# Kernel tuning notes

Measured on AMD Instinct MI355X. Metric: run time of the kernel, lower is better.

## Reference

```python
import jax, jax.numpy as jnp
import numpy as np

# Faithful JAX port of RayObsGraph.forward with T=1.
# torch_geometric GraphConv(x, edge_index) with add-aggregation and no edge
# weights computes: out[i] = lin_root(x[i]) + lin_rel(sum_{(j->i) in E} x[j]),
# where lin_root has no bias and lin_rel has a bias. dense_to_sparse(adj)
# yields an edge (row j -> col i) for every nonzero adj[j, i], so the
# aggregation equals binarize(adj)^T @ x, computed batched here instead of the
# original per-sample Python loop.

GS = 128      # graph_size
OBS = 1024    # obs_dim
H = 256       # gcn_h_size
OUT = 1024    # gcn_outsize
NO = 18       # num_outputs
B = 256

def setup_inputs() -> dict:
    key = jax.random.key(0)
    ks = jax.random.split(key, 16)
    inp = {
        "flat": jax.random.normal(ks[0], (B, OBS), jnp.float32),
        "nodes": jax.random.normal(ks[1], (B, GS, OBS), jnp.float32),
        "num_nodes": jax.random.randint(ks[2], (B,), 0, GS),
        "adj": jax.random.randint(ks[3], (B, GS, GS), 0, 2),
        "seq_lens": jnp.ones((B,), jnp.int32),
        # GraphConv 0: lin_rel (bias) + lin_root (no bias)
        "W0_rel": jax.random.normal(ks[4], (OBS, H), jnp.float32) / np.sqrt(OBS),
        "b0": jnp.zeros((H,), jnp.float32),
        "W0_root": jax.random.normal(ks[5], (OBS, H), jnp.float32) / np.sqrt(OBS),
        # GraphConv 1
        "W1_rel": jax.random.normal(ks[6], (H, OUT), jnp.float32) / np.sqrt(H),
        "b1": jnp.zeros((OUT,), jnp.float32),
        "W1_root": jax.random.normal(ks[7], (H, OUT), jnp.float32) / np.sqrt(H),
        # logit / value branches (SlimFC, activation None)
        "Wl": jax.random.normal(ks[8], (OUT, NO), jnp.float32) / np.sqrt(OUT),
        "bl": jnp.zeros((NO,), jnp.float32),
        "Wv": jax.random.normal(ks[9], (OUT, 1), jnp.float32) / np.sqrt(OUT),
        "bv": jnp.zeros((1,), jnp.float32),
    }
    return inp

def _forward(flat, nodes, adj, num_nodes,
             W0_rel, b0, W0_root, W1_rel, b1, W1_root, Wl, bl, Wv, bv):
    bsz = flat.shape[0]
    bi = jnp.arange(bsz)
    n = num_nodes
    nm1 = jnp.maximum(n - 1, 0)
    has_prev = n > 0

    # dense_to_sparse treats any nonzero entry as an edge (weight unused)
    A = (adj != 0).astype(flat.dtype)                       # [B, GS, GS]
    A = A.at[bi, n, n].set(1.0)
    A = A.at[bi, n, nm1].set(jnp.where(has_prev, 1.0, A[bi, n, nm1]))
    A = A.at[bi, nm1, n].set(jnp.where(has_prev, 1.0, A[bi, nm1, n]))

    # write current observation into node slot num_nodes
    x = nodes.at[bi, n].set(flat)                           # [B, GS, OBS]

    At = jnp.swapaxes(A, 1, 2)                              # message j->i: A^T
    aggr0 = jnp.einsum('bij,bjd->bid', At, x)               # [B, GS, OBS]
    h0 = jax.nn.relu(aggr0 @ W0_rel + b0 + x @ W0_root)     # [B, GS, H]
    aggr1 = jnp.einsum('bij,bjd->bid', At, h0)              # [B, GS, H]
    h1 = jax.nn.relu(aggr1 @ W1_rel + b1 + h0 @ W1_root)    # [B, GS, OUT]

    node_out = h1[bi, n]                                    # [B, OUT]
    logits = node_out @ Wl + bl                             # [B, NO]
    values = (node_out @ Wv + bv).squeeze(-1)               # [B]
    return logits, values

def reference(flat, nodes, num_nodes, adj, seq_lens,
              W0_rel, b0, W0_root, W1_rel, b1, W1_root, Wl, bl, Wv, bv):
    # seq_lens only determines B = len(seq_lens); T = flat.shape[0] // B = 1
    del seq_lens
    return _forward(flat, nodes, adj, num_nodes,
                    W0_rel, b0, W0_root, W1_rel, b1, W1_root, Wl, bl, Wv, bv)
```

## Files before the change

### kernel.cpp

```cpp
#include <hip/hip_runtime.h>
#include <hip/hip_bf16.h>
#include <cstdint>
#include <cstddef>

#define GS     128
#define OBS    1024
#define HSZ    256
#define OUTSZ  1024
#define NOUT   18
#define BATCH  256

typedef short  short8  __attribute__((ext_vector_type(8)));
typedef float  f32x4   __attribute__((ext_vector_type(4)));

__device__ __forceinline__ uint32_t f2bf_bits(float f) {
  uint32_t u = __builtin_bit_cast(uint32_t, f);
  return (u + 0x7fffu + ((u >> 16) & 1u)) >> 16;
}
__device__ __forceinline__ float bf_bits2f(uint32_t b) {
  return __builtin_bit_cast(float, b << 16);
}
__device__ __forceinline__ uint4 cvt8s(const float4 a, const float4 b) {
  float v[8] = {a.x, a.y, a.z, a.w, b.x, b.y, b.z, b.w};
  uint32_t h[8];
#pragma unroll
  for (int e = 0; e < 8; ++e) h[e] = f2bf_bits(v[e]);
  return make_uint4(h[0] | (h[1] << 16), h[2] | (h[3] << 16),
                    h[4] | (h[5] << 16), h[6] | (h[7] << 16));
}

__device__ __forceinline__ void bar_lds() {
  asm volatile("s_waitcnt lgkmcnt(0)" ::: "memory");
  __builtin_amdgcn_s_barrier();
  __builtin_amdgcn_sched_barrier(0);
}

__global__ __launch_bounds__(256) void prep_kernel(
    const float* __restrict__ W0_rel, const float* __restrict__ W0_root,
    ushort* __restrict__ WtP,
    const float* __restrict__ W1_rel, const float* __restrict__ W1_root,
    ushort* __restrict__ W1bf)
{
  __shared__ float T[64][65];
  const int blk = blockIdx.x;
  const int t = threadIdx.x;
  if (blk < 128) {
    const int k0 = (blk & 15) * 64;
    const int n0 = (blk >> 4) * 64;
    for (int idx = t; idx < 4096; idx += 256) {
      const int r = idx >> 6, c = idx & 63;
      const int n = n0 + c;
      T[r][c] = (n < HSZ) ? W0_rel[(size_t)(k0 + r) * HSZ + n]
                          : W0_root[(size_t)(k0 + r) * HSZ + (n - HSZ)];
    }
    __syncthreads();
    for (int idx = t; idx < 512; idx += 256) {
      const int nl = idx >> 3;
      const int kc = idx & 7;
      uint32_t h[8];
#pragma unroll
      for (int e = 0; e < 8; ++e) h[e] = f2bf_bits(T[kc * 8 + e][nl]);
      const int kg = k0 + kc * 8;
      const uint4 w = make_uint4(h[0] | (h[1] << 16), h[2] | (h[3] << 16),
                                 h[4] | (h[5] << 16), h[6] | (h[7] << 16));
      *(uint4*)&WtP[((size_t)((kg >> 5) * 512 + n0 + nl)) * 32 + (kg & 31)] = w;
    }
  } else {
    const int base = (blk - 128) * 16384;
    for (int it = 0; it < 64; ++it) {
      const int idx = base + it * 256 + t;
      const int k = idx >> 10, o = idx & 1023;
      const float v = (k < HSZ) ? W1_rel[(size_t)k * OUTSZ + o]
                                : W1_root[(size_t)(k - HSZ) * OUTSZ + o];
      W1bf[idx] = (ushort)f2bf_bits(v);
    }
  }
}

__global__ __launch_bounds__(512, 2) void mega_kernel(
    const float* __restrict__ flat, const float* __restrict__ nodes,
    const int* __restrict__ num_nodes, const int* __restrict__ adj,
    const float* __restrict__ b0, const ushort* __restrict__ WtP,
    ushort* __restrict__ zbf)
{
  __shared__ alignas(16) char smem[135168];
  ushort (*Ys)[264]      = (ushort (*)[264])smem;
  ushort (*As2)[128][72] = (ushort (*)[128][72])smem;
  __shared__ uint32_t rm[128][4];
  __shared__ uint32_t cmL[128][4];

  const int b  = blockIdx.x;
  const int nb = num_nodes[b];
  const int t  = threadIdx.x;
  const int wv = t >> 6, lane = t & 63;
  const int ln = lane & 15, q = lane >> 4;

  {
    const int* abase = adj + ((size_t)b * GS + wv * 16) * GS;
    int va[16], vb[16];
#pragma unroll
    for (int i = 0; i < 16; ++i) {
      va[i] = abase[i * GS + lane];
      vb[i] = abase[i * GS + 64 + lane];
    }
#pragma unroll
    for (int i = 0; i < 16; ++i) {
      const int k = wv * 16 + i;
      const unsigned long long m0 = __ballot(va[i] != 0);
      const unsigned long long m1 = __ballot(vb[i] != 0);
      if (lane == 0) {
        rm[k][0] = (uint32_t)m0; rm[k][1] = (uint32_t)(m0 >> 32);
        rm[k][2] = (uint32_t)m1; rm[k][3] = (uint32_t)(m1 >> 32);
      }
    }
  }
  __syncthreads();
  if (t < 128) {
    uint32_t c0 = 0, c1 = 0, c2 = 0, c3 = 0;
    const int w = t >> 5, sh = t & 31;
#pragma unroll 8
    for (int k = 0; k < 128; ++k) {
      const uint32_t bit = (rm[k][w] >> sh) & 1u;
      if (k < 32)      c0 |= bit << k;
      else if (k < 64) c1 |= bit << (k - 32);
      else if (k < 96) c2 |= bit << (k - 64);
      else             c3 |= bit << (k - 96);
    }
    cmL[t][0] = c0; cmL[t][1] = c1; cmL[t][2] = c2; cmL[t][3] = c3;
  }
  __syncthreads();
  if (t == 0) {
    cmL[nb][nb >> 5] |= 1u << (nb & 31);
    if (nb > 0) {
      cmL[nb - 1][nb >> 5] |= 1u << (nb & 31);
      cmL[nb][(nb - 1) >> 5] |= 1u << ((nb - 1) & 31);
    }
  }

  const int arow = t >> 2;
  const int akb  = (t & 3) * 16;
  const float* xsrc = ((arow == nb) ? (flat + (size_t)b * OBS)
                                    : (nodes + ((size_t)b * GS + arow) * OBS)) + akb;
  const ushort* bptr = WtP + ((size_t)(wv * 64 + ln)) * 32 + q * 8;

  f32x4 acc[4][8] = {};

  {
    const float4 a0 = *(const float4*)(xsrc);
    const float4 a1 = *(const float4*)(xsrc + 4);
    const float4 a2 = *(const float4*)(xsrc + 8);
    const float4 a3 = *(const float4*)(xsrc + 12);
    *(uint4*)&As2[0][arow][akb]     = cvt8s(a0, a1);
    *(uint4*)&As2[0][arow][akb + 8] = cvt8s(a2, a3);
  }
  float4 g0 = *(const float4*)(xsrc + 64);
  float4 g1 = *(const float4*)(xsrc + 68);
  float4 g2 = *(const float4*)(xsrc + 72);
  float4 g3 = *(const float4*)(xsrc + 76);
  short8 bA0 = *(const short8*)(bptr);
  short8 bA1 = *(const short8*)(bptr + 512);
  short8 bA2 = *(const short8*)(bptr + 1024);
  short8 bA3 = *(const short8*)(bptr + 1536);
  bar_lds();

  for (int s = 0; s < 16; ++s) {
    const int buf = s & 1;
    const ushort* bpB = bptr + ((size_t)(2 * s + 1)) * 16384;
    const short8 bB0 = *(const short8*)(bpB);
    const short8 bB1 = *(const short8*)(bpB + 512);
    const short8 bB2 = *(const short8*)(bpB + 1024);
    const short8 bB3 = *(const short8*)(bpB + 1536);
    short8 ah[8];
#pragma unroll
    for (int ii = 0; ii < 8; ++ii)
      ah[ii] = *(const short8*)&As2[buf][ii * 16 + ln][q * 8];
#pragma unroll
    for (int ii = 0; ii < 8; ++ii) {
      acc[0][ii] = __builtin_amdgcn_mfma_f32_16x16x32_bf16(bA0, ah[ii], acc[0][ii], 0, 0, 0);
      acc[1][ii] = __builtin_amdgcn_mfma_f32_16x16x32_bf16(bA1, ah[ii], acc[1][ii], 0, 0, 0);
      acc[2][ii] = __builtin_amdgcn_mfma_f32_16x16x32_bf16(bA2, ah[ii], acc[2][ii], 0, 0, 0);
      acc[3][ii] = __builtin_amdgcn_mfma_f32_16x16x32_bf16(bA3, ah[ii], acc[3][ii], 0, 0, 0);
    }
    short8 ah2[8];
#pragma unroll
    for (int ii = 0; ii < 8; ++ii)
      ah2[ii] = *(const short8*)&As2[buf][ii * 16 + ln][32 + q * 8];
    if (s + 1 < 16) {
      *(uint4*)&As2[buf ^ 1][arow][akb]     = cvt8s(g0, g1);
      *(uint4*)&As2[buf ^ 1][arow][akb + 8] = cvt8s(g2, g3);
    }
    short8 nA0 = {}, nA1 = {}, nA2 = {}, nA3 = {};
    if (s + 1 < 16) {
      const ushort* bpA = bptr + ((size_t)(2 * s + 2)) * 16384;
      nA0 = *(const short8*)(bpA);
      nA1 = *(const short8*)(bpA + 512);
      nA2 = *(const short8*)(bpA + 1024);
      nA3 = *(const short8*)(bpA + 1536);
    }
    if (s + 2 < 16) {
      g0 = *(const float4*)(xsrc + (s + 2) * 64);
      g1 = *(const float4*)(xsrc + (s + 2) * 64 + 4);
      g2 = *(const float4*)(xsrc + (s + 2) * 64 + 8);
      g3 = *(const float4*)(xsrc + (s + 2) * 64 + 12);
    }
#pragma unroll
    for (int ii = 0; ii < 8; ++ii) {
      acc[0][ii] = __builtin_amdgcn_mfma_f32_16x16x32_bf16(bB0, ah2[ii], acc[0][ii], 0, 0, 0);
      acc[1][ii] = __builtin_amdgcn_mfma_f32_16x16x32_bf16(bB1, ah2[ii], acc[1][ii], 0, 0, 0);
      acc[2][ii] = __builtin_amdgcn_mfma_f32_16x16x32_bf16(bB2, ah2[ii], acc[2][ii], 0, 0, 0);
      acc[3][ii] = __builtin_amdgcn_mfma_f32_16x16x32_bf16(bB3, ah2[ii], acc[3][ii], 0, 0, 0);
    }
    bA0 = nA0; bA1 = nA1; bA2 = nA2; bA3 = nA3;
    bar_lds();
  }

#pragma unroll
  for (int jj = 0; jj < 4; ++jj) {
    const int cat = wv * 64 + jj * 16 + q * 4;
    const int h   = cat & 255;
    const int kof = (cat < 256) ? 0 : 128;
#pragma unroll
    for (int ii = 0; ii < 8; ++ii) {
      const int kk = kof + ii * 16 + ln;
#pragma unroll
      for (int r = 0; r < 4; ++r)
        Ys[h + r][kk] = (ushort)f2bf_bits(acc[jj][ii][r]);
    }
  }
  __syncthreads();

  f32x4 acc2[8][2] = {};
#pragma unroll
  for (int ks = 0; ks < 4; ++ks) {
    const short8 bf0 = *(const short8*)&Ys[wv * 32 + ln][ks * 32 + q * 8];
    const short8 bf1 = *(const short8*)&Ys[wv * 32 + 16 + ln][ks * 32 + q * 8];
#pragma unroll
    for (int jt = 0; jt < 8; ++jt) {
      const uint32_t w = cmL[jt * 16 + ln][ks];
      const uint32_t byte_ = (w >> (q * 8)) & 0xFFu;
      short8 af;
#pragma unroll
      for (int i = 0; i < 8; ++i)
        af[i] = (short)(((byte_ >> i) & 1u) ? 0x3F80 : 0);
      acc2[jt][0] = __builtin_amdgcn_mfma_f32_16x16x32_bf16(af, bf0, acc2[jt][0], 0, 0, 0);
      acc2[jt][1] = __builtin_amdgcn_mfma_f32_16x16x32_bf16(af, bf1, acc2[jt][1], 0, 0, 0);
    }
  }

  const uint32_t S0 = cmL[nb][0], S1 = cmL[nb][1],
                 S2 = cmL[nb][2], S3 = cmL[nb][3];
  const int hl0 = wv * 32 + ln, hl1 = hl0 + 16;
  const float bb0 = b0[hl0];
  const float bb1 = b0[hl1];

  float asum0 = 0.f, asum1 = 0.f;
#pragma unroll
  for (int jt = 0; jt < 8; ++jt)
#pragma unroll
    for (int r = 0; r < 4; ++r) {
      const int j = jt * 16 + q * 4 + r;
      const uint32_t Sw = (j < 32) ? S0 : (j < 64) ? S1 : (j < 96) ? S2 : S3;
      const bool sj = (Sw >> (j & 31)) & 1u;
      const bool isn = (j == nb);
      {
        const float yroot = bf_bits2f(Ys[hl0][128 + j]);
        const float v = fmaxf(bb0 + yroot + acc2[jt][0][r], 0.f);
        if (sj) asum0 += v;
        if (isn) zbf[(size_t)b * 512 + 256 + hl0] = (ushort)f2bf_bits(v);
      }
      {
        const float yroot = bf_bits2f(Ys[hl1][128 + j]);
        const float v = fmaxf(bb1 + yroot + acc2[jt][1][r], 0.f);
        if (sj) asum1 += v;
        if (isn) zbf[(size_t)b * 512 + 256 + hl1] = (ushort)f2bf_bits(v);
      }
    }
  asum0 += __shfl_down(asum0, 32);
  asum0 += __shfl_down(asum0, 16);
  asum1 += __shfl_down(asum1, 32);
  asum1 += __shfl_down(asum1, 16);
  if (q == 0) {
    zbf[(size_t)b * 512 + hl0] = (ushort)f2bf_bits(asum0);
    zbf[(size_t)b * 512 + hl1] = (ushort)f2bf_bits(asum1);
  }
}

__global__ __launch_bounds__(256) void d_kernel(
    const ushort* __restrict__ zbf, const ushort* __restrict__ W1bf,
    const float* __restrict__ b1, const float* __restrict__ Wl,
    const float* __restrict__ Wv, const float* __restrict__ bl,
    const float* __restrict__ bv, float* __restrict__ out)
{
  __shared__ float a1s[256];
  __shared__ float rns[256];
  __shared__ float pl[19][4];
  const int b = blockIdx.x, t = threadIdx.x;
  const int wv = t >> 6, lane = t & 63;

  a1s[t] = bf_bits2f(zbf[(size_t)b * 512 + t]);
  rns[t] = bf_bits2f(zbf[(size_t)b * 512 + 256 + t]);
  __syncthreads();

  const int o4 = t * 4;
  float4 a = *(const float4*)&b1[o4];
  const ushort* wp = W1bf + o4;
#pragma unroll 8
  for (int k = 0; k < 256; ++k) {
    const ushort4 w4 = *(const ushort4*)(wp + (size_t)k * OUTSZ);
    const float s = a1s[k];
    a.x = fmaf(s, bf_bits2f(w4.x), a.x);
    a.y = fmaf(s, bf_bits2f(w4.y), a.y);
    a.z = fmaf(s, bf_bits2f(w4.z), a.z);
    a.w = fmaf(s, bf_bits2f(w4.w), a.w);
  }
#pragma unroll 8
  for (int k = 0; k < 256; ++k) {
    const ushort4 w4 = *(const ushort4*)(wp + (size_t)(256 + k) * OUTSZ);
    const float s = rns[k];
    a.x = fmaf(s, bf_bits2f(w4.x), a.x);
    a.y = fmaf(s, bf_bits2f(w4.y), a.y);
    a.z = fmaf(s, bf_bits2f(w4.z), a.z);
    a.w = fmaf(s, bf_bits2f(w4.w), a.w);
  }
  const float av[4] = {fmaxf(a.x, 0.f), fmaxf(a.y, 0.f),
                       fmaxf(a.z, 0.f), fmaxf(a.w, 0.f)};

  float p[19];
#pragma unroll
  for (int c = 0; c < 19; ++c) {
    float s = 0.f;
#pragma unroll
    for (int j = 0; j < 4; ++j) {
      const float w = (c < NOUT) ? Wl[(size_t)(o4 + j) * NOUT + c] : Wv[o4 + j];
      s = fmaf(av[j], w, s);
    }
    p[c] = s;
  }
#pragma unroll
  for (int c = 0; c < 19; ++c) {
    float v = p[c];
    v += __shfl_down(v, 32); v += __shfl_down(v, 16);
    v += __shfl_down(v, 8);  v += __shfl_down(v, 4);
    v += __shfl_down(v, 2);  v += __shfl_down(v, 1);
    if (lane == 0) pl[c][wv] = v;
  }
  __syncthreads();
  if (t < 19) {
    const float s = pl[t][0] + pl[t][1] + pl[t][2] + pl[t][3];
    if (t < NOUT) out[(size_t)b * NOUT + t] = s + bl[t];
    else          out[(size_t)BATCH * NOUT + b] = s + bv[0];
  }
}

extern "C" void kernel_launch(void* const* d_in, const int* in_sizes, int n_in,
                              void* d_out, int out_size, void* d_ws, size_t ws_size,
                              hipStream_t stream)
{
  const float* flat      = (const float*)d_in[0];
  const float* nodes     = (const float*)d_in[1];
  const int*   num_nodes = (const int*)  d_in[2];
  const int*   adj       = (const int*)  d_in[3];
  const float* W0_rel    = (const float*)d_in[5];
  const float* b0        = (const float*)d_in[6];
  const float* W0_root   = (const float*)d_in[7];
  const float* W1_rel    = (const float*)d_in[8];
  const float* b1        = (const float*)d_in[9];
  const float* W1_root   = (const float*)d_in[10];
  const float* Wl        = (const float*)d_in[11];
  const float* bl        = (const float*)d_in[12];
  const float* Wv        = (const float*)d_in[13];
  const float* bv        = (const float*)d_in[14];
  float* out = (float*)d_out;

  char* ws = (char*)d_ws;
  ushort* WtP  = (ushort*)ws;  ws += (size_t)512 * OBS * 2;
  ushort* W1bf = (ushort*)ws;  ws += (size_t)512 * OUTSZ * 2;
  ushort* zbf  = (ushort*)ws;  ws += (size_t)BATCH * 512 * 2;

  prep_kernel<<<160, 256, 0, stream>>>(
      W0_rel, W0_root, WtP, W1_rel, W1_root, W1bf);
  mega_kernel<<<BATCH, 512, 0, stream>>>(
      flat, nodes, num_nodes, adj, b0, WtP, zbf);
  d_kernel<<<BATCH, 256, 0, stream>>>(
      zbf, W1bf, b1, Wl, Wv, bl, bv, out);
}
```

Measured before the change: 308.8 us.

## Split mega_kernel per sample across two 256-thread blocks by hidden half

Each batch sample now runs on two blocks of 256 threads, each computing half of the 256 hidden units (matching rel and root weight columns), which doubles the grid and cuts shared memory per block roughly in half. Each wave keeps its own private Y tile, so the block-wide barrier before the adjacency MFMA is replaced by a local LDS wait. The cost is that both blocks reload and convert the full node feature matrix and adjacency per sample, doubling that global traffic.

```diff
diff --git a/kernel.cpp b/kernel.cpp
--- a/kernel.cpp
+++ b/kernel.cpp
@@ -77,26 +77,28 @@
   }
 }
 
-__global__ __launch_bounds__(512, 2) void mega_kernel(
+__global__ __launch_bounds__(256, 2) void mega_kernel(
     const float* __restrict__ flat, const float* __restrict__ nodes,
     const int* __restrict__ num_nodes, const int* __restrict__ adj,
     const float* __restrict__ b0, const ushort* __restrict__ WtP,
     ushort* __restrict__ zbf)
 {
-  __shared__ alignas(16) char smem[135168];
-  ushort (*Ys)[264]      = (ushort (*)[264])smem;
-  ushort (*As2)[128][72] = (ushort (*)[128][72])smem;
+  __shared__ alignas(16) char smem[67584];
+  ushort (*Yp)[2][32][132] = (ushort (*)[2][32][132])smem;
+  ushort (*As2)[128][72]   = (ushort (*)[128][72])smem;
   __shared__ uint32_t rm[128][4];
   __shared__ uint32_t cmL[128][4];
 
-  const int b  = blockIdx.x;
+  const int bx = blockIdx.x;
+  const int b  = bx >> 1;
+  const int hh = bx & 1;
   const int nb = num_nodes[b];
   const int t  = threadIdx.x;
   const int wv = t >> 6, lane = t & 63;
   const int ln = lane & 15, q = lane >> 4;
 
   {
-    const int* abase = adj + ((size_t)b * GS + wv * 16) * GS;
+    const int* abase = adj + ((size_t)b * GS + wv * 32) * GS;
     int va[16], vb[16];
 #pragma unroll
     for (int i = 0; i < 16; ++i) {
@@ -105,7 +107,22 @@
     }
 #pragma unroll
     for (int i = 0; i < 16; ++i) {
-      const int k = wv * 16 + i;
+      const int k = wv * 32 + i;
+      const unsigned long long m0 = __ballot(va[i] != 0);
+      const unsigned long long m1 = __ballot(vb[i] != 0);
+      if (lane == 0) {
+        rm[k][0] = (uint32_t)m0; rm[k][1] = (uint32_t)(m0 >> 32);
+        rm[k][2] = (uint32_t)m1; rm[k][3] = (uint32_t)(m1 >> 32);
+      }
+    }
+#pragma unroll
+    for (int i = 0; i < 16; ++i) {
+      va[i] = abase[(16 + i) * GS + lane];
+      vb[i] = abase[(16 + i) * GS + 64 + lane];
+    }
+#pragma unroll
+    for (int i = 0; i < 16; ++i) {
+      const int k = wv * 32 + 16 + i;
       const unsigned long long m0 = __ballot(va[i] != 0);
       const unsigned long long m1 = __ballot(vb[i] != 0);
       if (lane == 0) {
@@ -137,11 +154,12 @@
     }
   }
 
-  const int arow = t >> 2;
-  const int akb  = (t & 3) * 16;
+  const int arow = t >> 1;
+  const int akb  = (t & 1) * 32;
   const float* xsrc = ((arow == nb) ? (flat + (size_t)b * OBS)
                                     : (nodes + ((size_t)b * GS + arow) * OBS)) + akb;
-  const ushort* bptr = WtP + ((size_t)(wv * 64 + ln)) * 32 + q * 8;
+  const ushort* bp_rel  = WtP + ((size_t)(hh * 128 + wv * 32 + ln)) * 32 + q * 8;
+  const ushort* bp_root = WtP + ((size_t)(256 + hh * 128 + wv * 32 + ln)) * 32 + q * 8;
 
   f32x4 acc[4][8] = {};
 
@@ -150,26 +168,36 @@
     const float4 a1 = *(const float4*)(xsrc + 4);
     const float4 a2 = *(const float4*)(xsrc + 8);
     const float4 a3 = *(const float4*)(xsrc + 12);
-    *(uint4*)&As2[0][arow][akb]     = cvt8s(a0, a1);
-    *(uint4*)&As2[0][arow][akb + 8] = cvt8s(a2, a3);
+    const float4 a4 = *(const float4*)(xsrc + 16);
+    const float4 a5 = *(const float4*)(xsrc + 20);
+    const float4 a6 = *(const float4*)(xsrc + 24);
+    const float4 a7 = *(const float4*)(xsrc + 28);
+    *(uint4*)&As2[0][arow][akb]      = cvt8s(a0, a1);
+    *(uint4*)&As2[0][arow][akb + 8]  = cvt8s(a2, a3);
+    *(uint4*)&As2[0][arow][akb + 16] = cvt8s(a4, a5);
+    *(uint4*)&As2[0][arow][akb + 24] = cvt8s(a6, a7);
   }
   float4 g0 = *(const float4*)(xsrc + 64);
   float4 g1 = *(const float4*)(xsrc + 68);
   float4 g2 = *(const float4*)(xsrc + 72);
   float4 g3 = *(const float4*)(xsrc + 76);
-  short8 bA0 = *(const short8*)(bptr);
-  short8 bA1 = *(const short8*)(bptr + 512);
-  short8 bA2 = *(const short8*)(bptr + 1024);
-  short8 bA3 = *(const short8*)(bptr + 1536);
+  float4 g4 = *(const float4*)(xsrc + 80);
+  float4 g5 = *(const float4*)(xsrc + 84);
+  float4 g6 = *(const float4*)(xsrc + 88);
+  float4 g7 = *(const float4*)(xsrc + 92);
+  short8 bA0 = *(const short8*)(bp_rel);
+  short8 bA1 = *(const short8*)(bp_rel + 512);
+  short8 bA2 = *(const short8*)(bp_root);
+  short8 bA3 = *(const short8*)(bp_root + 512);
   bar_lds();
 
   for (int s = 0; s < 16; ++s) {
     const int buf = s & 1;
-    const ushort* bpB = bptr + ((size_t)(2 * s + 1)) * 16384;
-    const short8 bB0 = *(const short8*)(bpB);
-    const short8 bB1 = *(const short8*)(bpB + 512);
-    const short8 bB2 = *(const short8*)(bpB + 1024);
-    const short8 bB3 = *(const short8*)(bpB + 1536);
+    const size_t sb = (size_t)(2 * s + 1) * 16384;
+    const short8 bB0 = *(const short8*)(bp_rel + sb);
+    const short8 bB1 = *(const short8*)(bp_rel + sb + 512);
+    const short8 bB2 = *(const short8*)(bp_root + sb);
+    const short8 bB3 = *(const short8*)(bp_root + sb + 512);
     short8 ah[8];
 #pragma unroll
     for (int ii = 0; ii < 8; ++ii)
@@ -186,22 +214,17 @@
     for (int ii = 0; ii < 8; ++ii)
       ah2[ii] = *(const short8*)&As2[buf][ii * 16 + ln][32 + q * 8];
     if (s + 1 < 16) {
-      *(uint4*)&As2[buf ^ 1][arow][akb]     = cvt8s(g0, g1);
-      *(uint4*)&As2[buf ^ 1][arow][akb + 8] = cvt8s(g2, g3);
-    }
-    short8 nA0 = {}, nA1 = {}, nA2 = {}, nA3 = {};
-    if (s + 1 < 16) {
-      const ushort* bpA = bptr + ((size_t)(2 * s + 2)) * 16384;
-      nA0 = *(const short8*)(bpA);
-      nA1 = *(const short8*)(bpA + 512);
-      nA2 = *(const short8*)(bpA + 1024);
-      nA3 = *(const short8*)(bpA + 1536);
+      *(uint4*)&As2[buf ^ 1][arow][akb]      = cvt8s(g0, g1);
+      *(uint4*)&As2[buf ^ 1][arow][akb + 8]  = cvt8s(g2, g3);
+      *(uint4*)&As2[buf ^ 1][arow][akb + 16] = cvt8s(g4, g5);
+      *(uint4*)&As2[buf ^ 1][arow][akb + 24] = cvt8s(g6, g7);
     }
     if (s + 2 < 16) {
-      g0 = *(const float4*)(xsrc + (s + 2) * 64);
-      g1 = *(const float4*)(xsrc + (s + 2) * 64 + 4);
-      g2 = *(const float4*)(xsrc + (s + 2) * 64 + 8);
-      g3 = *(const float4*)(xsrc + (s + 2) * 64 + 12);
+      const float* xp = xsrc + (s + 2) * 64;
+      g0 = *(const float4*)(xp);      g1 = *(const float4*)(xp + 4);
+      g2 = *(const float4*)(xp + 8);  g3 = *(const float4*)(xp + 12);
+      g4 = *(const float4*)(xp + 16); g5 = *(const float4*)(xp + 20);
+      g6 = *(const float4*)(xp + 24); g7 = *(const float4*)(xp + 28);
     }
 #pragma unroll
     for (int ii = 0; ii < 8; ++ii) {
@@ -210,30 +233,36 @@
       acc[2][ii] = __builtin_amdgcn_mfma_f32_16x16x32_bf16(bB2, ah2[ii], acc[2][ii], 0, 0, 0);
       acc[3][ii] = __builtin_amdgcn_mfma_f32_16x16x32_bf16(bB3, ah2[ii], acc[3][ii], 0, 0, 0);
     }
-    bA0 = nA0; bA1 = nA1; bA2 = nA2; bA3 = nA3;
+    if (s + 1 < 16) {
+      const size_t sa = (size_t)(2 * s + 2) * 16384;
+      bA0 = *(const short8*)(bp_rel + sa);
+      bA1 = *(const short8*)(bp_rel + sa + 512);
+      bA2 = *(const short8*)(bp_root + sa);
+      bA3 = *(const short8*)(bp_root + sa + 512);
+    }
     bar_lds();
   }
 
 #pragma unroll
   for (int jj = 0; jj < 4; ++jj) {
-    const int cat = wv * 64 + jj * 16 + q * 4;
-    const int h   = cat & 255;
-    const int kof = (cat < 256) ? 0 : 128;
+    const int side = jj >> 1;
+    const int hb   = (jj & 1) * 16 + q * 4;
 #pragma unroll
     for (int ii = 0; ii < 8; ++ii) {
-      const int kk = kof + ii * 16 + ln;
+      const int node = ii * 16 + ln;
 #pragma unroll
       for (int r = 0; r < 4; ++r)
-        Ys[h + r][kk] = (ushort)f2bf_bits(acc[jj][ii][r]);
-    }
-  }
-  __syncthreads();
+        Yp[wv][side][hb + r][node] = (ushort)f2bf_bits(acc[jj][ii][r]);
+    }
+  }
+  asm volatile("s_waitcnt lgkmcnt(0)" ::: "memory");
+  __builtin_amdgcn_sched_barrier(0);
 
   f32x4 acc2[8][2] = {};
 #pragma unroll
   for (int ks = 0; ks < 4; ++ks) {
-    const short8 bf0 = *(const short8*)&Ys[wv * 32 + ln][ks * 32 + q * 8];
-    const short8 bf1 = *(const short8*)&Ys[wv * 32 + 16 + ln][ks * 32 + q * 8];
+    const short8 bf0 = *(const short8*)&Yp[wv][0][ln][ks * 32 + q * 8];
+    const short8 bf1 = *(const short8*)&Yp[wv][0][16 + ln][ks * 32 + q * 8];
 #pragma unroll
     for (int jt = 0; jt < 8; ++jt) {
       const uint32_t w = cmL[jt * 16 + ln][ks];
@@ -249,9 +278,10 @@
 
   const uint32_t S0 = cmL[nb][0], S1 = cmL[nb][1],
                  S2 = cmL[nb][2], S3 = cmL[nb][3];
-  const int hl0 = wv * 32 + ln, hl1 = hl0 + 16;
-  const float bb0 = b0[hl0];
-  const float bb1 = b0[hl1];
+  const int hg0 = hh * 128 + wv * 32 + ln;
+  const int hg1 = hg0 + 16;
+  const float bb0 = b0[hg0];
+  const float bb1 = b0[hg1];
 
   float asum0 = 0.f, asum1 = 0.f;
 #pragma unroll
@@ -263,16 +293,16 @@
       const bool sj = (Sw >> (j & 31)) & 1u;
       const bool isn = (j == nb);
       {
-        const float yroot = bf_bits2f(Ys[hl0][128 + j]);
+        const float yroot = bf_bits2f(Yp[wv][1][ln][j]);
         const float v = fmaxf(bb0 + yroot + acc2[jt][0][r], 0.f);
         if (sj) asum0 += v;
-        if (isn) zbf[(size_t)b * 512 + 256 + hl0] = (ushort)f2bf_bits(v);
+        if (isn) zbf[(size_t)b * 512 + 256 + hg0] = (ushort)f2bf_bits(v);
       }
       {
-        const float yroot = bf_bits2f(Ys[hl1][128 + j]);
+        const float yroot = bf_bits2f(Yp[wv][1][16 + ln][j]);
         const float v = fmaxf(bb1 + yroot + acc2[jt][1][r], 0.f);
         if (sj) asum1 += v;
-        if (isn) zbf[(size_t)b * 512 + 256 + hl1] = (ushort)f2bf_bits(v);
+        if (isn) zbf[(size_t)b * 512 + 256 + hg1] = (ushort)f2bf_bits(v);
       }
     }
   asum0 += __shfl_down(asum0, 32);
@@ -280,8 +310,8 @@
   asum1 += __shfl_down(asum1, 32);
   asum1 += __shfl_down(asum1, 16);
   if (q == 0) {
-    zbf[(size_t)b * 512 + hl0] = (ushort)f2bf_bits(asum0);
-    zbf[(size_t)b * 512 + hl1] = (ushort)f2bf_bits(asum1);
+    zbf[(size_t)b * 512 + hg0] = (ushort)f2bf_bits(asum0);
+    zbf[(size_t)b * 512 + hg1] = (ushort)f2bf_bits(asum1);
   }
 }
 
@@ -379,7 +409,7 @@
 
   prep_kernel<<<160, 256, 0, stream>>>(
       W0_rel, W0_root, WtP, W1_rel, W1_root, W1bf);
-  mega_kernel<<<BATCH, 512, 0, stream>>>(
+  mega_kernel<<<2 * BATCH, 256, 0, stream>>>(
       flat, nodes, num_nodes, adj, b0, WtP, zbf);
   d_kernel<<<BATCH, 256, 0, stream>>>(
       zbf, W1bf, b1, Wl, Wv, bl, bv, out);
```

Result: slower. 324.8 us (+5.2%).
